# Kernel tuning notes

Hardware: AMD Instinct MI355X
Metric: run time of the kernel (lower is better)

## Reference

```python
import jax, jax.numpy as jnp
import numpy as np

T, B, INP = 64, 4, 768
Q = E = 384  # hidden // divisor = 1536 // 4
DFF = 2 * INP


def _binop(ei, ej):
    # masked associative operator for the linear recurrence s_t = f_t*s_{t-1}+c_t
    ui, xi, mi = ei
    uj, xj, mj = ej
    cond = mj > 0
    return (jnp.where(cond, uj, uj * ui),
            jnp.where(cond, xj, uj * xi + xj),
            jnp.where(cond, mj, mi))


def setup_inputs() -> dict:
    key = jax.random.key(0)
    ks = jax.random.split(key, 10)
    n = lambda i, shp: jax.random.normal(ks[i], shp, jnp.float32)
    inp = n(0, (T, B, INP))
    is_first = (jax.random.uniform(ks[1], (T, B, 1)) < 0.05).astype(jnp.float32)
    drops = jnp.ones((T, B, 1), jnp.float32)            # eval-mode dropout mask
    init_inp = jnp.zeros((B, INP), jnp.float32)
    init_state = jnp.zeros((B, Q * E), jnp.float32)
    return {
        'inp': inp, 'is_first': is_first, 'drops': drops,
        'init_inp': init_inp, 'init_state': init_state,
        'mix_mu': jax.random.uniform(ks[2], (INP,), jnp.float32),
        'mix_W': n(3, (INP, Q)) / np.sqrt(INP),
        'layer_W': n(4, (INP, 2 * Q + 2 * E)) / np.sqrt(INP),
        'proj_W': n(5, (E, INP)) / np.sqrt(E),
        'rms_w': jnp.ones((E,), jnp.float32),
        'ln_w': jnp.ones((INP,), jnp.float32),
        'ln_b': jnp.zeros((INP,), jnp.float32),
        'ffn_W1': n(6, (INP, DFF)) / np.sqrt(INP),
        'ffn_W2': n(7, (INP, DFF)) / np.sqrt(INP),
        'ffn_W3': n(8, (DFF, INP)) / np.sqrt(DFF),
    }


def reference(inp, is_first, drops, init_inp, init_state, mix_mu, mix_W,
              layer_W, proj_W, rms_w, ln_w, ln_b, ffn_W1, ffn_W2, ffn_W3):
    Tt, Bb, _ = inp.shape
    Qd, Ed = mix_W.shape[1], proj_W.shape[0]
    init = init_state.reshape(Bb, Qd, Ed)[None]                 # [1,B,Q,E]
    init_masks = jnp.concatenate([jnp.ones_like(is_first[:1]), is_first[1:]], 0)
    lasts = jnp.concatenate([jnp.zeros_like(inp[:1]), inp[:-1]], 0)
    lasts = lasts + init_masks * (init_inp[None] - lasts)
    # components
    mixed = mix_mu * inp + (1.0 - mix_mu) * lasts               # MixingLayer
    forget = jax.nn.sigmoid(mixed @ mix_W)                      # [T,B,Q]
    forget = (forget - 1.0) * drops + 1.0
    parts = (inp @ layer_W) * drops                             # [T,B,2Q+2E]
    qk = jax.nn.elu(parts[..., :2 * Qd]) + 1.0
    query, keyv = qk[..., :Qd], qk[..., Qd:]
    reset, value = parts[..., 2 * Qd:2 * Qd + Ed], parts[..., 2 * Qd + Ed:]
    value = jax.nn.sigmoid(reset) * value
    cand = keyv[..., :, None] * value[..., None, :]             # [T,B,Q,E]
    forget_b = jnp.broadcast_to(forget[..., None], cand.shape)
    cands = cand + init_masks[..., None] * forget_b * init
    masks = jnp.broadcast_to(is_first[..., None], cand.shape)
    # masked log-depth parallel scan of s_t = f_t*s_{t-1} + c_t
    states = jax.lax.associative_scan(_binop, (forget_b, cands, masks), axis=0)[1]
    out = jnp.einsum('tbq,tbqe->tbe', query, states)            # query @ state
    out = out * jax.lax.rsqrt(jnp.mean(out * out, -1, keepdims=True) + 1e-6) * rms_w
    out = out @ proj_W                                          # [T,B,INP]
    # RNNCell: residual + LayerNorm + gated FFN (SwiGLU-style GatingLayer)
    h = inp + out
    mu = jnp.mean(h, -1, keepdims=True)
    var = jnp.var(h, -1, keepdims=True)
    h = (h - mu) * jax.lax.rsqrt(var + 1e-5) * ln_w + ln_b
    return (jax.nn.silu(h @ ffn_W1) * (h @ ffn_W2)) @ ffn_W3
```

## Files before the change

### kernel.cpp

```cpp
#include <hip/hip_runtime.h>
#include <hip/hip_bf16.h>

#define T_DIM 64
#define B_DIM 4
#define INP_D 768
#define Q_D   384
#define E_D   384
#define DFF_D 1536
#define NTOK  256

typedef short bf16x8 __attribute__((ext_vector_type(8)));
typedef float f32x4  __attribute__((ext_vector_type(4)));

__device__ __forceinline__ float sigf(float x)  { return 1.0f / (1.0f + __expf(-x)); }
__device__ __forceinline__ float elu1f(float x) { return x > 0.0f ? x + 1.0f : __expf(x); }

__device__ __forceinline__ short f2b(float x) {
  union { __hip_bfloat16 b; short s; } u;
  u.b = __float2bfloat16(x);
  return u.s;
}
__device__ __forceinline__ bf16x8 cvt8(float4 a, float4 b) {
  bf16x8 r;
  r[0] = f2b(a.x); r[1] = f2b(a.y); r[2] = f2b(a.z); r[3] = f2b(a.w);
  r[4] = f2b(b.x); r[5] = f2b(b.y); r[6] = f2b(b.z); r[7] = f2b(b.w);
  return r;
}

#define WS_FORGET 0
#define WS_QUERY  98304
#define WS_KEYV   196608
#define WS_VALUE  294912
#define WS_PATT   393216
#define WS_HPRE   1179648
#define WS_BF     1376256
#define PB_INP   0
#define PB_MIXED 196608
#define PB_ATTN  393216
#define PB_H     491520
#define PB_G     688128
#define PK_MIX   1081344
#define PK_LAYER 1376256
#define PK_PROJ  2555904
#define PK_W1    2850816
#define PK_W2    4030464
#define PK_W3    5210112

__global__ __launch_bounds__(256) void k_conv(const float* __restrict__ inp,
                                              const float* __restrict__ is_first,
                                              const float* __restrict__ init_inp,
                                              const float* __restrict__ mu,
                                              const float* __restrict__ mixW,
                                              const float* __restrict__ layerW,
                                              const float* __restrict__ projW,
                                              const float* __restrict__ W1,
                                              const float* __restrict__ W2,
                                              const float* __restrict__ W3,
                                              short* __restrict__ wsb) {
  const int blk = blockIdx.x;
  const int tid = threadIdx.x;
  if (blk >= 2592) {
    if (blk < 2688) {
      const int idx = (blk - 2592) * 2048 + tid * 8;
      float4 a = *(const float4*)&inp[idx], b = *(const float4*)&inp[idx + 4];
      *(bf16x8*)&wsb[PB_INP + idx] = cvt8(a, b);
    } else {
      const int idx = (blk - 2688) * 2048 + tid * 8;
      const int c = idx % INP_D, tok = idx / INP_D;
      const int t = tok >> 2, b = tok & 3;
      const float fr = (t == 0) ? 1.0f : is_first[tok];
      const float* lastp = (fr > 0.5f) ? &init_inp[b * INP_D + c] : &inp[idx - 4 * INP_D];
      float4 x0 = *(const float4*)&inp[idx], x1 = *(const float4*)&inp[idx + 4];
      float4 l0 = *(const float4*)&lastp[0], l1 = *(const float4*)&lastp[4];
      float4 m0 = *(const float4*)&mu[c],    m1 = *(const float4*)&mu[c + 4];
      float4 r0, r1;
      r0.x = m0.x * x0.x + (1.0f - m0.x) * l0.x;
      r0.y = m0.y * x0.y + (1.0f - m0.y) * l0.y;
      r0.z = m0.z * x0.z + (1.0f - m0.z) * l0.z;
      r0.w = m0.w * x0.w + (1.0f - m0.w) * l0.w;
      r1.x = m1.x * x1.x + (1.0f - m1.x) * l1.x;
      r1.y = m1.y * x1.y + (1.0f - m1.y) * l1.y;
      r1.z = m1.z * x1.z + (1.0f - m1.z) * l1.z;
      r1.w = m1.w * x1.w + (1.0f - m1.w) * l1.w;
      *(bf16x8*)&wsb[PB_MIXED + idx] = cvt8(r0, r1);
    }
    return;
  }
  const float* src; short* dst; int N, kb, nb64;
  if (blk < 144)        { src = mixW;   dst = wsb + PK_MIX;   N = 384;  int r = blk;        kb = r / 6;  nb64 = r % 6; }
  else if (blk < 720)   { src = layerW; dst = wsb + PK_LAYER; N = 1536; int r = blk - 144;  kb = r / 24; nb64 = r % 24; }
  else if (blk < 864)   { src = projW;  dst = wsb + PK_PROJ;  N = 768;  int r = blk - 720;  kb = r / 12; nb64 = r % 12; }
  else if (blk < 1440)  { src = W1;     dst = wsb + PK_W1;    N = 1536; int r = blk - 864;  kb = r / 24; nb64 = r % 24; }
  else if (blk < 2016)  { src = W2;     dst = wsb + PK_W2;    N = 1536; int r = blk - 1440; kb = r / 24; nb64 = r % 24; }
  else                  { src = W3;     dst = wsb + PK_W3;    N = 768;  int r = blk - 2016; kb = r / 12; nb64 = r % 12; }

  __shared__ float lds[32][68];
  {
    const int r = tid >> 3, c8 = (tid & 7) * 8;
    const float* p = &src[(size_t)(kb * 32 + r) * N + nb64 * 64 + c8];
    *(float4*)&lds[r][c8]     = *(const float4*)p;
    *(float4*)&lds[r][c8 + 4] = *(const float4*)(p + 4);
  }
  __syncthreads();
  {
    const int nb = tid >> 6, lane = tid & 63, g = lane >> 4, c = lane & 15;
    unsigned int w[4];
#pragma unroll
    for (int jj = 0; jj < 4; ++jj) {
      unsigned short lo = (unsigned short)f2b(lds[g * 8 + jj * 2][nb * 16 + c]);
      unsigned short hi = (unsigned short)f2b(lds[g * 8 + jj * 2 + 1][nb * 16 + c]);
      w[jj] = (unsigned int)lo | ((unsigned int)hi << 16);
    }
    const int N16 = N >> 4;
    size_t o = ((size_t)kb * N16 + (nb64 * 4 + nb)) * 512 + lane * 8;
    uint4 pk; pk.x = w[0]; pk.y = w[1]; pk.z = w[2]; pk.w = w[3];
    *(uint4*)&dst[o] = pk;
  }
}

template<int KSTEPS, int SUBT, bool DUAL, int ASTRIDE>
__device__ __forceinline__ void mm_core(const short* __restrict__ Arow, int kg,
                                        const short* __restrict__ B1, int bn1, int N16a,
                                        const short* __restrict__ B2, int bn2, int N16b,
                                        int lane, f32x4* acc1, f32x4* acc2) {
  bf16x8 a_c = *(const bf16x8*)&Arow[kg];
  bf16x8 b1c[SUBT], b2c[SUBT];
#pragma unroll
  for (int s = 0; s < SUBT; ++s)
    b1c[s] = *(const bf16x8*)&B1[((size_t)(bn1 + s)) * 512 + lane * 8];
  if constexpr (DUAL) {
#pragma unroll
    for (int s = 0; s < SUBT; ++s)
      b2c[s] = *(const bf16x8*)&B2[((size_t)(bn2 + s)) * 512 + lane * 8];
  }
#pragma unroll 2
  for (int kb = 0; kb < KSTEPS; ++kb) {
    bf16x8 a_n = a_c;
    bf16x8 b1n[SUBT], b2n[SUBT];
    if (kb + 1 < KSTEPS) {
      a_n = *(const bf16x8*)&Arow[(kb + 1) * 32 + kg];
#pragma unroll
      for (int s = 0; s < SUBT; ++s)
        b1n[s] = *(const bf16x8*)&B1[((size_t)(kb + 1) * N16a + bn1 + s) * 512 + lane * 8];
      if constexpr (DUAL) {
#pragma unroll
        for (int s = 0; s < SUBT; ++s)
          b2n[s] = *(const bf16x8*)&B2[((size_t)(kb + 1) * N16b + bn2 + s) * 512 + lane * 8];
      }
    }
#pragma unroll
    for (int s = 0; s < SUBT; ++s)
      acc1[s] = __builtin_amdgcn_mfma_f32_16x16x32_bf16(a_c, b1c[s], acc1[s], 0, 0, 0);
    if constexpr (DUAL) {
#pragma unroll
      for (int s = 0; s < SUBT; ++s)
        acc2[s] = __builtin_amdgcn_mfma_f32_16x16x32_bf16(a_c, b2c[s], acc2[s], 0, 0, 0);
    }
    a_c = a_n;
#pragma unroll
    for (int s = 0; s < SUBT; ++s) b1c[s] = b1n[s];
    if constexpr (DUAL) {
#pragma unroll
      for (int s = 0; s < SUBT; ++s) b2c[s] = b2n[s];
    }
  }
}

#define WAVE_SETUP  const int tid = threadIdx.x, w = tid >> 6, l = tid & 63; \
                    const int m0 = blockIdx.x * 64; \
                    const int rowA = m0 + w * 16 + (l & 15); \
                    const int kg = (l >> 4) * 8; (void)kg;

__global__ __launch_bounds__(256) void k_qkvfg(const short* __restrict__ inp_bf,
                                               const short* __restrict__ mixed_bf,
                                               const short* __restrict__ Mixp,
                                               const short* __restrict__ Lp,
                                               const float* __restrict__ drops,
                                               float* __restrict__ forget,
                                               float* __restrict__ query,
                                               float* __restrict__ keyv,
                                               float* __restrict__ value) {
  WAVE_SETUP
  const int y = blockIdx.y;
  if (y < 12) {
    const int n0 = y * 32, bn = y * 2;
    const short* Arow = &mixed_bf[(size_t)rowA * INP_D];
    f32x4 acc[2] = {(f32x4){0.f,0.f,0.f,0.f}, (f32x4){0.f,0.f,0.f,0.f}};
    mm_core<24, 2, false, INP_D>(Arow, kg, Mixp, bn, 24, nullptr, 0, 0, l, acc, nullptr);
#pragma unroll
    for (int i = 0; i < 4; ++i) {
      const int row = m0 + w * 16 + ((l >> 4) << 2) + i;
      const float d = drops[row];
#pragma unroll
      for (int s = 0; s < 2; ++s) {
        const int col = n0 + s * 16 + (l & 15);
        forget[(size_t)row * Q_D + col] = (sigf(acc[s][i]) - 1.0f) * d + 1.0f;
      }
    }
    return;
  }
  const short* Arow = &inp_bf[(size_t)rowA * INP_D];
  if (y < 36) {
    const bool isq = (y < 24);
    const int yy = isq ? y - 12 : y - 24;
    float* dst = isq ? query : keyv;
    const int bn = (isq ? 0 : 24) + yy * 2;
    f32x4 acc[2] = {(f32x4){0.f,0.f,0.f,0.f}, (f32x4){0.f,0.f,0.f,0.f}};
    mm_core<24, 2, false, INP_D>(Arow, kg, Lp, bn, 96, nullptr, 0, 0, l, acc, nullptr);
#pragma unroll
    for (int i = 0; i < 4; ++i) {
      const int row = m0 + w * 16 + ((l >> 4) << 2) + i;
      const float d = drops[row];
#pragma unroll
      for (int s = 0; s < 2; ++s) {
        const int col = yy * 32 + s * 16 + (l & 15);
        dst[(size_t)row * Q_D + col] = elu1f(acc[s][i] * d);
      }
    }
  } else {
    const int q = y - 36;
    const int bn_r = 48 + q * 2, bn_v = 72 + q * 2;
    f32x4 a1[2] = {(f32x4){0.f,0.f,0.f,0.f}, (f32x4){0.f,0.f,0.f,0.f}};
    f32x4 a2[2] = {(f32x4){0.f,0.f,0.f,0.f}, (f32x4){0.f,0.f,0.f,0.f}};
    mm_core<24, 2, true, INP_D>(Arow, kg, Lp, bn_r, 96, Lp, bn_v, 96, l, a1, a2);
#pragma unroll
    for (int i = 0; i < 4; ++i) {
      const int row = m0 + w * 16 + ((l >> 4) << 2) + i;
      const float d = drops[row];
#pragma unroll
      for (int s = 0; s < 2; ++s) {
        const int col = q * 32 + s * 16 + (l & 15);
        value[(size_t)row * E_D + col] = sigf(a1[s][i] * d) * (a2[s][i] * d);
      }
    }
  }
}

__global__ __launch_bounds__(256) void k_proj(const short* __restrict__ attn_bf,
                                              const short* __restrict__ Bp,
                                              const float* __restrict__ inp,
                                              float* __restrict__ hpre) {
  WAVE_SETUP
  const int n0 = blockIdx.y * 32, bn = blockIdx.y * 2;
  const short* Arow = &attn_bf[(size_t)rowA * E_D];
  f32x4 acc[2] = {(f32x4){0.f,0.f,0.f,0.f}, (f32x4){0.f,0.f,0.f,0.f}};
  mm_core<12, 2, false, E_D>(Arow, kg, Bp, bn, 48, nullptr, 0, 0, l, acc, nullptr);
#pragma unroll
  for (int i = 0; i < 4; ++i) {
    const int row = m0 + w * 16 + ((l >> 4) << 2) + i;
#pragma unroll
    for (int s = 0; s < 2; ++s) {
      const int col = n0 + s * 16 + (l & 15);
      hpre[(size_t)row * INP_D + col] = acc[s][i] + inp[(size_t)row * INP_D + col];
    }
  }
}

__global__ __launch_bounds__(256) void k_ffn(const short* __restrict__ h_bf,
                                             const short* __restrict__ W1p,
                                             const short* __restrict__ W2p,
                                             short* __restrict__ g_bf) {
  WAVE_SETUP
  const int n0 = blockIdx.y * 32, bn = blockIdx.y * 2;
  const short* Arow = &h_bf[(size_t)rowA * INP_D];
  f32x4 a1[2] = {(f32x4){0.f,0.f,0.f,0.f}, (f32x4){0.f,0.f,0.f,0.f}};
  f32x4 a2[2] = {(f32x4){0.f,0.f,0.f,0.f}, (f32x4){0.f,0.f,0.f,0.f}};
  mm_core<24, 2, true, INP_D>(Arow, kg, W1p, bn, 96, W2p, bn, 96, l, a1, a2);
#pragma unroll
  for (int i = 0; i < 4; ++i) {
    const int row = m0 + w * 16 + ((l >> 4) << 2) + i;
#pragma unroll
    for (int s = 0; s < 2; ++s) {
      const int col = n0 + s * 16 + (l & 15);
      const float v1 = a1[s][i], v2 = a2[s][i];
      g_bf[(size_t)row * DFF_D + col] = f2b(v1 * sigf(v1) * v2);
    }
  }
}

__global__ __launch_bounds__(256) void k_out(const short* __restrict__ g_bf,
                                             const short* __restrict__ Bp,
                                             float* __restrict__ out) {
  WAVE_SETUP
  const int n0 = blockIdx.y * 32, bn = blockIdx.y * 2;
  const short* Arow = &g_bf[(size_t)rowA * DFF_D];
  f32x4 acc[2] = {(f32x4){0.f,0.f,0.f,0.f}, (f32x4){0.f,0.f,0.f,0.f}};
  mm_core<48, 2, false, DFF_D>(Arow, kg, Bp, bn, 48, nullptr, 0, 0, l, acc, nullptr);
#pragma unroll
  for (int i = 0; i < 4; ++i) {
    const int row = m0 + w * 16 + ((l >> 4) << 2) + i;
#pragma unroll
    for (int s = 0; s < 2; ++s) {
      const int col = n0 + s * 16 + (l & 15);
      out[(size_t)row * INP_D + col] = acc[s][i];
    }
  }
}

__global__ __launch_bounds__(256) void k_scan(const float* __restrict__ forget,
                                              const float* __restrict__ query,
                                              const float* __restrict__ keyv,
                                              const float* __restrict__ value,
                                              const float* __restrict__ is_first,
                                              const float* __restrict__ init_state,
                                              float* __restrict__ patt) {
  __shared__ float stg[2][144];
  __shared__ float pacc[2][256];
  const int tid = threadIdx.x;
  const int e  = blockIdx.x * 64 + (tid & 63);
  const int qg = tid >> 6;
  const int qc = blockIdx.y;
  const int b  = blockIdx.z;
  const int q0 = qc * 48 + qg * 12;

  float s[12], ini[12];
#pragma unroll
  for (int j = 0; j < 12; ++j) {
    ini[j] = init_state[((size_t)b * Q_D + q0 + j) * E_D + e];
    s[j]   = ini[j];
  }

  auto stageld = [&](int tok) -> float {
    const int which = tid / 48, o = tid % 48;
    const float* src = which == 0 ? forget : (which == 1 ? keyv : query);
    return src[(size_t)tok * Q_D + qc * 48 + o];
  };

  float v_c, if_c;
  if (tid < 144) stg[0][tid] = stageld(b);
  v_c  = value[(size_t)b * E_D + e];
  if_c = 0.0f;
  __syncthreads();

  for (int t = 0; t < T_DIM; ++t) {
    const int tok = t * B_DIM + b;
    const int cur = t & 1;
    float stage_n = 0.0f, v_n = 0.0f, if_n = 0.0f;
    if (t + 1 < T_DIM) {
      const int tok1 = tok + B_DIM;
      if (tid < 144) stage_n = stageld(tok1);
      v_n  = value[(size_t)tok1 * E_D + e];
      if_n = is_first[tok1];
    }
    if (if_c > 0.5f) {
#pragma unroll
      for (int j = 0; j < 12; ++j) s[j] = ini[j];
    }
    const float4* f4 = (const float4*)&stg[cur][qg * 12];
    const float4* k4 = (const float4*)&stg[cur][48 + qg * 12];
    const float4* q4 = (const float4*)&stg[cur][96 + qg * 12];
    float p = 0.0f;
#pragma unroll
    for (int jj = 0; jj < 3; ++jj) {
      const float4 fv = f4[jj], kv = k4[jj], qv = q4[jj];
#pragma unroll
      for (int j2 = 0; j2 < 4; ++j2) {
        const int sj = jj * 4 + j2;
        s[sj] = fmaf((&fv.x)[j2], s[sj], (&kv.x)[j2] * v_c);
        p     = fmaf((&qv.x)[j2], s[sj], p);
      }
    }
    pacc[cur][tid] = p;
    if (t + 1 < T_DIM && tid < 144) stg[cur ^ 1][tid] = stage_n;
    __syncthreads();
    if (tid < 64) {
      float r = pacc[cur][tid] + pacc[cur][tid + 64] + pacc[cur][tid + 128] + pacc[cur][tid + 192];
      patt[((size_t)qc * NTOK + tok) * E_D + blockIdx.x * 64 + tid] = r;
    }
    v_c  = v_n;
    if_c = if_n;
  }
}

__global__ __launch_bounds__(128) void ep_rms(const float* __restrict__ patt,
                                              const float* __restrict__ rms_w,
                                              short* __restrict__ attn_bf) {
  const int tok = blockIdx.x, tid = threadIdx.x;
  float x[3], ss = 0.0f;
#pragma unroll
  for (int i = 0; i < 3; ++i) {
    const int e = i * 128 + tid;
    float a = 0.0f;
#pragma unroll
    for (int qc = 0; qc < 8; ++qc) a += patt[((size_t)qc * NTOK + tok) * E_D + e];
    x[i] = a;
    ss = fmaf(a, a, ss);
  }
#pragma unroll
  for (int off = 32; off; off >>= 1) ss += __shfl_down(ss, off, 64);
  __shared__ float r[2];
  const int wid = tid >> 6, lane = tid & 63;
  if (lane == 0) r[wid] = ss;
  __syncthreads();
  ss = r[0] + r[1];
  const float sc = rsqrtf(ss * (1.0f / E_D) + 1e-6f);
#pragma unroll
  for (int i = 0; i < 3; ++i) {
    const int e = i * 128 + tid;
    attn_bf[(size_t)tok * E_D + e] = f2b(x[i] * sc * rms_w[e]);
  }
}

__global__ __launch_bounds__(256) void ep_ln(const float* __restrict__ hpre,
                                             const float* __restrict__ ln_w,
                                             const float* __restrict__ ln_b,
                                             short* __restrict__ h_bf) {
  const int tok = blockIdx.x, tid = threadIdx.x;
  float x[3], s1 = 0.0f, s2 = 0.0f;
#pragma unroll
  for (int i = 0; i < 3; ++i) {
    x[i] = hpre[(size_t)tok * INP_D + i * 256 + tid];
    s1 += x[i];
    s2 = fmaf(x[i], x[i], s2);
  }
#pragma unroll
  for (int off = 32; off; off >>= 1) {
    s1 += __shfl_down(s1, off, 64);
    s2 += __shfl_down(s2, off, 64);
  }
  __shared__ float r1[4], r2[4];
  const int wid = tid >> 6, lane = tid & 63;
  if (lane == 0) { r1[wid] = s1; r2[wid] = s2; }
  __syncthreads();
  s1 = r1[0] + r1[1] + r1[2] + r1[3];
  s2 = r2[0] + r2[1] + r2[2] + r2[3];
  const float mean = s1 * (1.0f / INP_D);
  const float var  = s2 * (1.0f / INP_D) - mean * mean;
  const float sc   = rsqrtf(var + 1e-5f);
#pragma unroll
  for (int i = 0; i < 3; ++i) {
    const int c = i * 256 + tid;
    h_bf[(size_t)tok * INP_D + c] = f2b((x[i] - mean) * sc * ln_w[c] + ln_b[c]);
  }
}

extern "C" void kernel_launch(void* const* d_in, const int* in_sizes, int n_in,
                              void* d_out, int out_size, void* d_ws, size_t ws_size,
                              hipStream_t stream) {
  (void)in_sizes; (void)n_in; (void)out_size; (void)ws_size;
  const float* inp        = (const float*)d_in[0];
  const float* is_first   = (const float*)d_in[1];
  const float* drops      = (const float*)d_in[2];
  const float* init_inp   = (const float*)d_in[3];
  const float* init_state = (const float*)d_in[4];
  const float* mix_mu     = (const float*)d_in[5];
  const float* mix_W      = (const float*)d_in[6];
  const float* layer_W    = (const float*)d_in[7];
  const float* proj_W     = (const float*)d_in[8];
  const float* rms_w      = (const float*)d_in[9];
  const float* ln_w       = (const float*)d_in[10];
  const float* ln_b       = (const float*)d_in[11];
  const float* W1         = (const float*)d_in[12];
  const float* W2         = (const float*)d_in[13];
  const float* W3         = (const float*)d_in[14];
  float* out = (float*)d_out;
  float* ws  = (float*)d_ws;
  short* wsb = (short*)(ws + WS_BF);

  float* forget = ws + WS_FORGET;
  float* query  = ws + WS_QUERY;
  float* keyv   = ws + WS_KEYV;
  float* value  = ws + WS_VALUE;
  float* patt   = ws + WS_PATT;
  float* hpre   = ws + WS_HPRE;

  k_conv<<<2784, 256, 0, stream>>>(inp, is_first, init_inp, mix_mu,
                                   mix_W, layer_W, proj_W, W1, W2, W3, wsb);
  k_qkvfg<<<dim3(4, 48), 256, 0, stream>>>(wsb + PB_INP, wsb + PB_MIXED,
                                           wsb + PK_MIX, wsb + PK_LAYER, drops,
                                           forget, query, keyv, value);
  k_scan<<<dim3(6, 8, 4), 256, 0, stream>>>(forget, query, keyv, value,
                                            is_first, init_state, patt);
  ep_rms<<<NTOK, 128, 0, stream>>>(patt, rms_w, wsb + PB_ATTN);
  k_proj<<<dim3(4, 24), 256, 0, stream>>>(wsb + PB_ATTN, wsb + PK_PROJ, inp, hpre);
  ep_ln<<<NTOK, 256, 0, stream>>>(hpre, ln_w, ln_b, wsb + PB_H);
  k_ffn<<<dim3(4, 48), 256, 0, stream>>>(wsb + PB_H, wsb + PK_W1, wsb + PK_W2, wsb + PB_G);
  k_out<<<dim3(4, 24), 256, 0, stream>>>(wsb + PB_G, wsb + PK_W3, out);
}
```

Baseline: 198.7 us.

## Restructure scan into single-wave blocks with register prefetch and shuffle reduction

```diff
diff --git a/kernel.cpp b/kernel.cpp
--- a/kernel.cpp
+++ b/kernel.cpp
@@ -297,21 +297,20 @@
   }
 }
 
-__global__ __launch_bounds__(256) void k_scan(const float* __restrict__ forget,
-                                              const float* __restrict__ query,
-                                              const float* __restrict__ keyv,
-                                              const float* __restrict__ value,
-                                              const float* __restrict__ is_first,
-                                              const float* __restrict__ init_state,
-                                              float* __restrict__ patt) {
-  __shared__ float stg[2][144];
-  __shared__ float pacc[2][256];
-  const int tid = threadIdx.x;
-  const int e  = blockIdx.x * 64 + (tid & 63);
-  const int qg = tid >> 6;
-  const int qc = blockIdx.y;
-  const int b  = blockIdx.z;
-  const int q0 = qc * 48 + qg * 12;
+__global__ __launch_bounds__(64) void k_scan(const float* __restrict__ forget,
+                                             const float* __restrict__ query,
+                                             const float* __restrict__ keyv,
+                                             const float* __restrict__ value,
+                                             const float* __restrict__ is_first,
+                                             const float* __restrict__ init_state,
+                                             float* __restrict__ patt) {
+  const int lane = threadIdx.x;
+  const int et   = blockIdx.x;
+  const int qc   = blockIdx.y;
+  const int b    = blockIdx.z;
+  const int e    = et * 16 + (lane & 15);
+  const int qsub = lane >> 4;
+  const int q0   = qc * 48 + qsub * 12;
 
   float s[12], ini[12];
 #pragma unroll
@@ -320,56 +319,61 @@
     s[j]   = ini[j];
   }
 
-  auto stageld = [&](int tok) -> float {
-    const int which = tid / 48, o = tid % 48;
-    const float* src = which == 0 ? forget : (which == 1 ? keyv : query);
-    return src[(size_t)tok * Q_D + qc * 48 + o];
-  };
-
-  float v_c, if_c;
-  if (tid < 144) stg[0][tid] = stageld(b);
-  v_c  = value[(size_t)b * E_D + e];
-  if_c = 0.0f;
-  __syncthreads();
+  float4 f0[3], k0[3], qv0[3]; float v0, fi0;
+  float4 f1[3], k1[3], qv1[3]; float v1, fi1;
+
+#define SCAN_LD(tok, F, K, QV, V, FI, first)                                 \
+  {                                                                          \
+    const float* fp = &forget[(size_t)(tok) * Q_D + q0];                     \
+    const float* kp = &keyv  [(size_t)(tok) * Q_D + q0];                     \
+    const float* qp = &query [(size_t)(tok) * Q_D + q0];                     \
+    F[0] = *(const float4*)&fp[0]; F[1] = *(const float4*)&fp[4]; F[2] = *(const float4*)&fp[8]; \
+    K[0] = *(const float4*)&kp[0]; K[1] = *(const float4*)&kp[4]; K[2] = *(const float4*)&kp[8]; \
+    QV[0] = *(const float4*)&qp[0]; QV[1] = *(const float4*)&qp[4]; QV[2] = *(const float4*)&qp[8]; \
+    V = value[(size_t)(tok) * E_D + e];                                      \
+    FI = (first) ? 0.0f : is_first[tok];                                     \
+  }
+
+  SCAN_LD(b, f0, k0, qv0, v0, fi0, true);
+  SCAN_LD(B_DIM + b, f1, k1, qv1, v1, fi1, false);
 
   for (int t = 0; t < T_DIM; ++t) {
     const int tok = t * B_DIM + b;
-    const int cur = t & 1;
-    float stage_n = 0.0f, v_n = 0.0f, if_n = 0.0f;
-    if (t + 1 < T_DIM) {
-      const int tok1 = tok + B_DIM;
-      if (tid < 144) stage_n = stageld(tok1);
-      v_n  = value[(size_t)tok1 * E_D + e];
-      if_n = is_first[tok1];
-    }
-    if (if_c > 0.5f) {
+    float4 fc0 = f0[0], fc1 = f0[1], fc2 = f0[2];
+    float4 kc0 = k0[0], kc1 = k0[1], kc2 = k0[2];
+    float4 qc0 = qv0[0], qc1 = qv0[1], qc2 = qv0[2];
+    const float vc = v0, fic = fi0;
+    f0[0] = f1[0]; f0[1] = f1[1]; f0[2] = f1[2];
+    k0[0] = k1[0]; k0[1] = k1[1]; k0[2] = k1[2];
+    qv0[0] = qv1[0]; qv0[1] = qv1[1]; qv0[2] = qv1[2];
+    v0 = v1; fi0 = fi1;
+    if (t + 2 < T_DIM) {
+      SCAN_LD((t + 2) * B_DIM + b, f1, k1, qv1, v1, fi1, false);
+    }
+
+    if (fic > 0.5f) {
 #pragma unroll
       for (int j = 0; j < 12; ++j) s[j] = ini[j];
     }
-    const float4* f4 = (const float4*)&stg[cur][qg * 12];
-    const float4* k4 = (const float4*)&stg[cur][48 + qg * 12];
-    const float4* q4 = (const float4*)&stg[cur][96 + qg * 12];
     float p = 0.0f;
-#pragma unroll
-    for (int jj = 0; jj < 3; ++jj) {
-      const float4 fv = f4[jj], kv = k4[jj], qv = q4[jj];
-#pragma unroll
-      for (int j2 = 0; j2 < 4; ++j2) {
-        const int sj = jj * 4 + j2;
-        s[sj] = fmaf((&fv.x)[j2], s[sj], (&kv.x)[j2] * v_c);
-        p     = fmaf((&qv.x)[j2], s[sj], p);
+    const float4 fr[3]  = {fc0, fc1, fc2};
+    const float4 kr[3]  = {kc0, kc1, kc2};
+    const float4 qr[3]  = {qc0, qc1, qc2};
+#pragma unroll
+    for (int r = 0; r < 3; ++r) {
+#pragma unroll
+      for (int j = 0; j < 4; ++j) {
+        const int sj = r * 4 + j;
+        s[sj] = fmaf((&fr[r].x)[j], s[sj], (&kr[r].x)[j] * vc);
+        p     = fmaf((&qr[r].x)[j], s[sj], p);
       }
     }
-    pacc[cur][tid] = p;
-    if (t + 1 < T_DIM && tid < 144) stg[cur ^ 1][tid] = stage_n;
-    __syncthreads();
-    if (tid < 64) {
-      float r = pacc[cur][tid] + pacc[cur][tid + 64] + pacc[cur][tid + 128] + pacc[cur][tid + 192];
-      patt[((size_t)qc * NTOK + tok) * E_D + blockIdx.x * 64 + tid] = r;
-    }
-    v_c  = v_n;
-    if_c = if_n;
-  }
+    p += __shfl_xor(p, 16, 64);
+    p += __shfl_xor(p, 32, 64);
+    if (lane < 16)
+      patt[((size_t)qc * NTOK + tok) * E_D + et * 16 + lane] = p;
+  }
+#undef SCAN_LD
 }
 
 __global__ __launch_bounds__(128) void ep_rms(const float* __restrict__ patt,
@@ -469,7 +473,7 @@
   k_qkvfg<<<dim3(4, 48), 256, 0, stream>>>(wsb + PB_INP, wsb + PB_MIXED,
                                            wsb + PK_MIX, wsb + PK_LAYER, drops,
                                            forget, query, keyv, value);
-  k_scan<<<dim3(6, 8, 4), 256, 0, stream>>>(forget, query, keyv, value,
+  k_scan<<<dim3(24, 8, 4), 64, 0, stream>>>(forget, query, keyv, value,
                                             is_first, init_state, patt);
   ep_rms<<<NTOK, 128, 0, stream>>>(patt, rms_w, wsb + PB_ATTN);
   k_proj<<<dim3(4, 24), 256, 0, stream>>>(wsb + PB_ATTN, wsb + PK_PROJ, inp, hpre);
```

After: 169.5 us. 1.17x faster.
